# Kernel optimization log

Hardware: AMD Instinct MI355X
Metric: run time of the kernel (lower is better)

The kernel has to match this reference:

```python
import jax, jax.numpy as jnp
import numpy as np

B, C, H, W = 8, 512, 64, 64


def conv3x3(x, w, b):
    # x: [B,C,H,W], w: [O,I,3,3], b: [O]; stride 1, padding 1 (SAME)
    y = jax.lax.conv_general_dilated(
        x, w, window_strides=(1, 1), padding='SAME',
        dimension_numbers=('NCHW', 'OIHW', 'NCHW'))
    return y + b[None, :, None, None]


def setup_inputs() -> dict:
    key = jax.random.key(0)
    ks = jax.random.split(key, 8)
    wscale = 1.0 / np.sqrt(C * 9)  # keep attention logits in a sane range
    x = jax.random.normal(ks[0], (B, C, H, W), dtype=jnp.float32)
    wq = jax.random.normal(ks[1], (C, C, 3, 3), dtype=jnp.float32) * wscale
    bq = jax.random.normal(ks[2], (C,), dtype=jnp.float32) * 0.01
    wk = jax.random.normal(ks[3], (C, C, 3, 3), dtype=jnp.float32) * wscale
    bk = jax.random.normal(ks[4], (C,), dtype=jnp.float32) * 0.01
    wv = jax.random.normal(ks[5], (C, C, 3, 3), dtype=jnp.float32) * wscale
    bv = jax.random.normal(ks[6], (C,), dtype=jnp.float32) * 0.01
    gamma = jax.random.normal(ks[7], (1,), dtype=jnp.float32)
    return {'x': x, 'wq': wq, 'bq': bq, 'wk': wk, 'bk': bk,
            'wv': wv, 'bv': bv, 'gamma': gamma}


def reference(x, wq, bq, wk, bk, wv, bv, gamma):
    b, c, h, w = x.shape
    n = h * w
    q = conv3x3(x, wq, bq).reshape(b, c, n)   # [B,C,N]
    k = conv3x3(x, wk, bk).reshape(b, c, n)   # [B,C,N]
    v = conv3x3(x, wv, bv).reshape(b, c, n)   # [B,C,N]
    # channel-wise attention: [B,C,N] x [B,N,C] -> [B,C,C]
    attn = jnp.einsum('bcn,bdn->bcd', q, k)
    attn = jax.nn.softmax(attn, axis=-1)
    out = jnp.einsum('bcd,bdn->bcn', attn, v).reshape(b, c, h, w)
    return gamma * out + x
```

## Files before the change

### kernel.cpp

```cpp
#include <hip/hip_runtime.h>
#include <stdint.h>

typedef __attribute__((ext_vector_type(8))) short bf16x8;
typedef __attribute__((ext_vector_type(4))) float f32x4;
typedef __attribute__((ext_vector_type(4))) int i32x4;
typedef __attribute__((ext_vector_type(8))) int i32x8;
typedef __attribute__((ext_vector_type(8))) unsigned short u16x8;
typedef __attribute__((ext_vector_type(4))) unsigned short u16x4;

#define DI static __device__ __forceinline__

constexpr int CB = 8;
constexpr int BCH = 4;
constexpr int CC = 512;
constexpr int CN = 4096;
constexpr int K1 = CC * 9;
constexpr int MR = 3 * CC;
constexpr int KSPL = 8;
constexpr size_t XSPLIT = (size_t)BCH * 66 * 66 * 512;

DI unsigned short f2bf(float f) {
  union { float f; uint32_t u; } v; v.f = f;
  uint32_t r = (v.u + 0x7FFFu + ((v.u >> 16) & 1u)) >> 16;
  return (unsigned short)r;
}
DI float bf2f(unsigned short h) {
  union { uint32_t u; float f; } v; v.u = ((uint32_t)h) << 16;
  return v.f;
}
DI unsigned char f2e4m3(float x) {
  union { float f; uint32_t u; } v; v.f = x;
  uint32_t sgn = (v.u >> 24) & 0x80u;
  float a = fabsf(x);
  if (a < 0.015625f) {
    int qi = (int)rintf(a * 512.f);
    return (unsigned char)(sgn | (uint32_t)qi);
  }
  int e = (int)((v.u >> 23) & 0xff) - 127;
  uint32_t m3 = (v.u >> 20) & 7u;
  uint32_t rest = v.u & 0xFFFFFu;
  if (rest > 0x80000u || (rest == 0x80000u && (m3 & 1u))) {
    if (++m3 == 8u) { m3 = 0; ++e; }
  }
  if (e > 8 || (e == 8 && m3 == 7u)) return (unsigned char)(sgn | 0x7Eu);
  return (unsigned char)(sgn | ((uint32_t)(e + 7) << 3) | m3);
}

DI void g2lds16(const void* g, void* l) {
  __builtin_amdgcn_global_load_lds((const __attribute__((address_space(1))) void*)g,
                                   (__attribute__((address_space(3))) void*)l, 16, 0, 0);
}
#define SBAR()  __builtin_amdgcn_s_barrier()
#define SCHED() __builtin_amdgcn_sched_barrier(0)

__global__ __launch_bounds__(256) void pad_zero(unsigned short* __restrict__ Xhi,
                                                unsigned char* __restrict__ X8) {
  int id = blockIdx.x * 256 + threadIdx.x;
  if (id >= 4 * 260 * 16) return;
  int t = id & 15;
  int pp = (id >> 4) % 260;
  int b = id / (260 * 16);
  int hh, ww;
  if (pp < 66)       { hh = 0;  ww = pp; }
  else if (pp < 132) { hh = 65; ww = pp - 66; }
  else if (pp < 196) { hh = pp - 131; ww = 0; }
  else               { hh = pp - 195; ww = 65; }
  size_t pix = (((size_t)b * 66 + hh) * 66 + ww) * 512 + (size_t)t * 32;
  const u16x8 z = {0, 0, 0, 0, 0, 0, 0, 0};
  *(u16x8*)&Xhi[pix] = z;  *(u16x8*)&Xhi[pix + 8] = z;
  *(u16x8*)&Xhi[pix + 16] = z;  *(u16x8*)&Xhi[pix + 24] = z;
  const i32x4 z4 = {0, 0, 0, 0};
  *(i32x4*)&X8[pix] = z4;  *(i32x4*)&X8[pix + 16] = z4;
  *(i32x4*)&X8[XSPLIT + pix] = z4;  *(i32x4*)&X8[XSPLIT + pix + 16] = z4;
}

__global__ __launch_bounds__(256) void prep_xpad(const float* __restrict__ x,
                                                 unsigned short* __restrict__ Xhi,
                                                 unsigned char* __restrict__ X8) {
  int tid = threadIdx.x;
  int w = tid & 63;
  int ccl = tid >> 6;
  int blk = blockIdx.x;
  int h = blk & 63;
  int ccg = (blk >> 6) & 15;
  int b = blk >> 10;
  int c0 = (ccg * 4 + ccl) * 8;
  const float* xp = x + ((size_t)b * CC) * CN + h * 64 + w;
  u16x8 hi;
  unsigned long long lo8 = 0, hi8 = 0;
#pragma unroll
  for (int j = 0; j < 8; ++j) {
    float v = xp[(size_t)(c0 + j) * CN];
    unsigned short h16 = f2bf(v);
    float vhi = bf2f(h16);
    hi[j] = f2bf(vhi * 128.f);
    lo8 |= (unsigned long long)f2e4m3((v - vhi) * 256.f) << (8 * j);
    hi8 |= (unsigned long long)f2e4m3(vhi) << (8 * j);
  }
  size_t pix = (((size_t)b * 66 + (h + 1)) * 66 + (w + 1)) * 512;
  *(u16x8*)&Xhi[pix + c0] = hi;
  *(unsigned long long*)&X8[pix + c0] = lo8;
  *(unsigned long long*)&X8[XSPLIT + pix + c0] = hi8;
}

__global__ __launch_bounds__(256) void prep_abig(
    const float* __restrict__ wq, const float* __restrict__ wk,
    const float* __restrict__ wv, const float* __restrict__ bq,
    const float* __restrict__ bk, const float* __restrict__ bv,
    unsigned short* __restrict__ Ahi, unsigned char* __restrict__ A8,
    float* __restrict__ bias) {
  unsigned id = blockIdx.x * 256 + threadIdx.x;
  int m = id / K1;
  int r = id - m * K1;
  int t = r >> 9;
  int c = r & 511;
  int ky = t / 3;
  int kx = t - ky * 3;
  size_t ip = (size_t)m * 9216 + r;
  if (m < 1024) {
    const float* wp = (m < 512) ? wq : wk;
    int mm = (m < 512) ? m : m - 512;
    float wval = wp[(((size_t)mm * 512 + c) * 3 + ky) * 3 + kx];
    float whi = bf2f(f2bf(wval));
    Ahi[id] = f2bf(whi * 128.f);
    A8[ip] = f2e4m3(whi * 64.f);
    A8[ip + 4608] = f2e4m3((wval - whi) * 16384.f);
  } else {
    float wval = wv[(((size_t)(m - 1024) * 512 + c) * 3 + ky) * 3 + kx];
    Ahi[id] = f2bf(wval * 128.f);
    A8[ip] = 0;
    A8[ip + 4608] = 0;
  }
  if (id < 1536) {
    int mm = (int)id;
    bias[mm] = (mm < 512) ? bq[mm] : (mm < 1024) ? bk[mm - 512] : bv[mm - 1024];
  }
}

__global__ __launch_bounds__(512, 2) void conv_k(
    const unsigned short* __restrict__ Ahi,
    const unsigned char* __restrict__ A8,
    const unsigned short* __restrict__ Xhi,
    const unsigned char* __restrict__ X8,
    const float* __restrict__ bias,
    unsigned short* __restrict__ Qhi, unsigned short* __restrict__ Qlo,
    unsigned short* __restrict__ Khi, unsigned short* __restrict__ Klo,
    unsigned short* __restrict__ Vt)
{
  __shared__ __align__(16) unsigned char smem[4 * 32768];
  const int tid = threadIdx.x;
  const int lane = tid & 63;
  const int wid = tid >> 6;
  const int wr = wid >> 2;
  const int wc = wid & 3;

  int orig = blockIdx.x;
  int xcd, nbl, m0;
  if (orig < 256) {
    xcd = orig & 7; int j = orig >> 3;
    nbl = j >> 2;
    m0 = (j & 3) * 256;
  } else {
    int o = orig - 256;
    xcd = o & 7; int j = o >> 3;
    nbl = j >> 2;
    m0 = 1024 + (j & 3) * 128;
  }
  const int nb = xcd * 8 + nbl;
  const int n0 = nb * 256;
  const int bidx = n0 >> 12;
  const int nl0 = n0 & (CN - 1);
  const int h0 = nl0 >> 6;

  const int srow = tid >> 2;
  const int scu = tid & 3;
  const int scuS = scu ^ ((srow >> 1) & 3);
  const int d8 = (scuS & 1) ? -16 : 16;
  const size_t pixOfs = (((size_t)(bidx * 66 + h0 + (srow >> 6))) * 66 + (srow & 63)) * 512;
  const unsigned short* gAh0 = Ahi + (size_t)(m0 + srow) * K1 + scuS * 8;
  const unsigned short* gAh1 = gAh0 + (size_t)128 * K1;
  const unsigned short* gBh0 = Xhi + pixOfs + scuS * 8;
  const unsigned short* gBh1 = gBh0 + (size_t)2 * 66 * 512;
  const unsigned char* gA80 = A8 + (size_t)(m0 + srow) * 9216 + scuS * 16;
  const unsigned char* gA81 = gA80 + (size_t)128 * 9216;
  const unsigned char* gB80 = X8 + pixOfs + scuS * 16;
  const unsigned char* gB81 = gB80 + (size_t)2 * 66 * 512;
  const int wofs = wid * 1024;

  int c0S = 0, kxS = 0, tapS = 0;
  size_t tapOfs = 0;
  auto stage1 = [&](int slot) {
    int aOfs = tapS * 512 + c0S;
    size_t bOfs = tapOfs + (size_t)c0S;
    unsigned char* lA = smem + slot * 32768 + wofs;
    unsigned char* lB = smem + slot * 32768 + 16384 + wofs;
    g2lds16(gAh0 + aOfs, lA);
    g2lds16(gAh1 + aOfs, lA + 8192);
    g2lds16(gBh0 + bOfs, lB);
    g2lds16(gBh1 + bOfs, lB + 8192);
    c0S += 32;
    if (c0S == 512) {
      c0S = 0; ++tapS;
      if (kxS == 2) { kxS = 0; tapOfs += (size_t)64 * 512; }
      else { ++kxS; tapOfs += 512; }
    }
  };
  auto stage1v = [&](int slot) {
    int aOfs = tapS * 512 + c0S;
    size_t bOfs = tapOfs + (size_t)c0S;
    unsigned char* lA = smem + slot * 32768 + wofs;
    unsigned char* lB = smem + slot * 32768 + 16384 + wofs;
    g2lds16(gAh0 + aOfs, lA);
    g2lds16(gBh0 + bOfs, lB);
    g2lds16(gBh1 + bOfs, lB + 8192);
    c0S += 32;
    if (c0S == 512) {
      c0S = 0; ++tapS;
      if (kxS == 2) { kxS = 0; tapOfs += (size_t)64 * 512; }
      else { ++kxS; tapOfs += 512; }
    }
  };
  int c8 = 0, kx8 = 0, tap8 = 0, s8 = 0;
  size_t tapOfs8 = 0;
  auto stage2 = [&](int slot) {
    int so = (slot & 1) ? d8 : 0;
    int aOfs = s8 * 4608 + tap8 * 512 + c8;
    size_t bOfs = (size_t)s8 * XSPLIT + tapOfs8 + (size_t)c8;
    unsigned char* lA = smem + slot * 32768 + wofs;
    unsigned char* lB = smem + slot * 32768 + 16384 + wofs;
    g2lds16(gA80 + aOfs + so, lA);
    g2lds16(gA81 + aOfs + so, lA + 8192);
    g2lds16(gB80 + bOfs + so, lB);
    g2lds16(gB81 + bOfs + so, lB + 8192);
    c8 += 64;
    if (c8 == 512) {
      c8 = 0; ++tap8;
      if (tap8 == 9) { tap8 = 0; kx8 = 0; tapOfs8 = 0; ++s8; }
      else if (kx8 == 2) { kx8 = 0; tapOfs8 += (size_t)64 * 512; }
      else { ++kx8; tapOfs8 += 512; }
    }
  };

  f32x4 acc[8][4];
  const f32x4 fz = {0.f, 0.f, 0.f, 0.f};
#pragma unroll
  for (int i = 0; i < 8; ++i)
#pragma unroll
    for (int j = 0; j < 4; ++j) acc[i][j] = fz;

  const int kq = (lane >> 4) * 16;
  int slotC, slotS, t2;

  if (m0 < 1024) {
    const int rA = wr * 128 + (lane & 15);
    const int rB = wc * 64 + (lane & 15);
    const int kqA = kq ^ (((rA >> 1) & 3) << 4);
    const int kqB = kq ^ (((rB >> 1) & 3) << 4);

    stage1(0);
    stage1(1);
    asm volatile("s_waitcnt vmcnt(4)" ::: "memory");
    SCHED(); SBAR(); SCHED();
    {
      bf16x8 afA[4], bfA[4], afB[4], bfB[4], af1[4];
#pragma unroll
      for (int mf = 0; mf < 4; ++mf)
        afA[mf] = *(const bf16x8*)(smem + (rA + mf * 16) * 64 + kqA);
#pragma unroll
      for (int nf = 0; nf < 4; ++nf)
        bfA[nf] = *(const bf16x8*)(smem + 16384 + (rB + nf * 16) * 64 + kqB);
      slotC = 0; slotS = 2; t2 = 2;

#define CONV_BF(CURA, CURB, NXTA, NXTB)                                       \
  {                                                                           \
    if (t2 < 144) {                                                           \
      stage1(slotS); slotS = (slotS + 1) & 3;                                 \
      asm volatile("s_waitcnt vmcnt(4)" ::: "memory");                        \
    } else {                                                                  \
      asm volatile("s_waitcnt vmcnt(0)" ::: "memory");                        \
    }                                                                         \
    SCHED(); SBAR(); SCHED();                                                 \
    const unsigned char* lA = smem + slotC * 32768;                           \
    const int slotN = (slotC + 1) & 3;                                        \
    const unsigned char* lAn = smem + slotN * 32768;                          \
    _Pragma("unroll")                                                         \
    for (int mf = 0; mf < 4; ++mf)                                            \
      af1[mf] = *(const bf16x8*)(lA + (rA + 64 + mf * 16) * 64 + kqA);        \
    __builtin_amdgcn_s_setprio(1);                                            \
    _Pragma("unroll")                                                         \
    for (int mf = 0; mf < 4; ++mf) {                                          \
      _Pragma("unroll")                                                       \
      for (int nf = 0; nf < 4; ++nf)                                          \
        acc[mf][nf] = __builtin_amdgcn_mfma_f32_16x16x32_bf16(                \
            CURA[mf], CURB[nf], acc[mf][nf], 0, 0, 0);                        \
    }                                                                         \
    __builtin_amdgcn_s_setprio(0);                                            \
    _Pragma("unroll")                                                         \
    for (int mf = 0; mf < 4; ++mf)                                            \
      NXTA[mf] = *(const bf16x8*)(lAn + (rA + mf * 16) * 64 + kqA);           \
    _Pragma("unroll")                                                         \
    for (int nf = 0; nf < 4; ++nf)                                            \
      NXTB[nf] = *(const bf16x8*)(lAn + 16384 + (rB + nf * 16) * 64 + kqB);   \
    __builtin_amdgcn_s_setprio(1);                                            \
    _Pragma("unroll")                                                         \
    for (int mf = 0; mf < 4; ++mf) {                                          \
      _Pragma("unroll")                                                       \
      for (int nf = 0; nf < 4; ++nf)                                          \
        acc[mf + 4][nf] = __builtin_amdgcn_mfma_f32_16x16x32_bf16(            \
            af1[mf], CURB[nf], acc[mf + 4][nf], 0, 0, 0);                     \
    }                                                                         \
    __builtin_amdgcn_s_setprio(0);                                            \
    slotC = slotN;                                                            \
    ++t2;                                                                     \
  }

      for (int t = 0; t < 144; t += 2) {
        CONV_BF(afA, bfA, afB, bfB)
        CONV_BF(afB, bfB, afA, bfA)
      }
#undef CONV_BF
    }

    stage2(0); stage2(1);
    SCHED(); SBAR(); SCHED();
    stage2(2); stage2(3);
    {
      const int gq = lane >> 4;
      const int slotByte = (gq >> 1) << 15;
      const int cb2 = (gq & 1) * 2;
      const int fx = (((lane & 15) >> 1) & 3) ^ (gq >> 1);
      const int bo0 = ((cb2 ^ fx) << 4);
      const int bo1 = (((cb2 + 1) ^ fx) << 4);
      const int aRow = wr * 128 + (lane & 15);
      const int bRow = wc * 64 + (lane & 15);
      i32x8 aF[4], bF[4];
      for (int p = 0; p < 72; ++p) {
        SCHED(); SBAR(); SCHED();
        if (p < 71) { asm volatile("s_waitcnt vmcnt(8)" ::: "memory"); }
        else        { asm volatile("s_waitcnt vmcnt(0)" ::: "memory"); }
        SCHED();
        const unsigned char* pbA = smem + ((p & 1) << 16) + slotByte + aRow * 64;
        const unsigned char* pbB = smem + ((p & 1) << 16) + slotByte + 16384 + bRow * 64;
#pragma unroll
        for (int t = 0; t < 4; ++t) {
          *(i32x4*)&bF[t] = *(const i32x4*)(pbB + t * 1024 + bo0);
          *((i32x4*)&bF[t] + 1) = *(const i32x4*)(pbB + t * 1024 + bo1);
        }
#pragma unroll
        for (int s = 0; s < 4; ++s) {
          *(i32x4*)&aF[s] = *(const i32x4*)(pbA + s * 1024 + bo0);
          *((i32x4*)&aF[s] + 1) = *(const i32x4*)(pbA + s * 1024 + bo1);
        }
        __builtin_amdgcn_s_setprio(1);
#pragma unroll
        for (int s = 0; s < 4; ++s)
#pragma unroll
          for (int t = 0; t < 4; ++t)
            acc[s][t] = __builtin_amdgcn_mfma_scale_f32_16x16x128_f8f6f4(
                aF[s], bF[t], acc[s][t], 0, 0, 0, 127, 0, 127);
        __builtin_amdgcn_s_setprio(0);
#pragma unroll
        for (int s = 0; s < 4; ++s) {
          *(i32x4*)&aF[s] = *(const i32x4*)(pbA + (4 + s) * 1024 + bo0);
          *((i32x4*)&aF[s] + 1) = *(const i32x4*)(pbA + (4 + s) * 1024 + bo1);
        }
        __builtin_amdgcn_s_setprio(1);
#pragma unroll
        for (int s = 0; s < 4; ++s)
#pragma unroll
          for (int t = 0; t < 4; ++t)
            acc[s + 4][t] = __builtin_amdgcn_mfma_scale_f32_16x16x128_f8f6f4(
                aF[s], bF[t], acc[s + 4][t], 0, 0, 0, 127, 0, 127);
        __builtin_amdgcn_s_setprio(0);
        SCHED(); SBAR(); SCHED();
        if (p + 2 < 72) { stage2(2 * (p & 1)); stage2(2 * (p & 1) + 1); }
      }
    }
  } else {
    const int rAv = wr * 64 + (lane & 15);
    const int rB = wc * 64 + (lane & 15);
    const int kqA = kq ^ (((rAv >> 1) & 3) << 4);
    const int kqB = kq ^ (((rB >> 1) & 3) << 4);

    stage1v(0);
    stage1v(1);
    asm volatile("s_waitcnt vmcnt(3)" ::: "memory");
    SCHED(); SBAR(); SCHED();
    bf16x8 afA[4], bfA[4], afB[4], bfB[4];
#pragma unroll
    for (int mf = 0; mf < 4; ++mf)
      afA[mf] = *(const bf16x8*)(smem + (rAv + mf * 16) * 64 + kqA);
#pragma unroll
    for (int nf = 0; nf < 4; ++nf)
      bfA[nf] = *(const bf16x8*)(smem + 16384 + (rB + nf * 16) * 64 + kqB);
    slotC = 0; slotS = 2; t2 = 2;

#define CONV_LV(CURA, CURB, NXTA, NXTB)                                       \
  {                                                                           \
    if (t2 < 144) {                                                           \
      stage1v(slotS); slotS = (slotS + 1) & 3;                                \
      asm volatile("s_waitcnt vmcnt(3)" ::: "memory");                        \
    } else {                                                                  \
      asm volatile("s_waitcnt vmcnt(0)" ::: "memory");                        \
    }                                                                         \
    SCHED(); SBAR(); SCHED();                                                 \
    const int slotN = (slotC + 1) & 3;                                        \
    const unsigned char* lAn = smem + slotN * 32768;                          \
    _Pragma("unroll")                                                         \
    for (int mf = 0; mf < 4; ++mf)                                            \
      NXTA[mf] = *(const bf16x8*)(lAn + (rAv + mf * 16) * 64 + kqA);          \
    _Pragma("unroll")                                                         \
    for (int nf = 0; nf < 4; ++nf)                                            \
      NXTB[nf] = *(const bf16x8*)(lAn + 16384 + (rB + nf * 16) * 64 + kqB);   \
    __builtin_amdgcn_s_setprio(1);                                            \
    _Pragma("unroll")                                                         \
    for (int mf = 0; mf < 4; ++mf) {                                          \
      _Pragma("unroll")                                                       \
      for (int nf = 0; nf < 4; ++nf)                                          \
        acc[mf][nf] = __builtin_amdgcn_mfma_f32_16x16x32_bf16(                \
            CURA[mf], CURB[nf], acc[mf][nf], 0, 0, 0);                        \
    }                                                                         \
    __builtin_amdgcn_s_setprio(0);                                            \
    slotC = slotN;                                                            \
    ++t2;                                                                     \
  }

    for (int t = 0; t < 144; t += 2) {
      CONV_LV(afA, bfA, afB, bfB)
      CONV_LV(afB, bfB, afA, bfA)
    }
#undef CONV_LV
  }

  constexpr float SC = 1.f / 16384.f;
  if (m0 < 1024) {
#pragma unroll
    for (int mf = 0; mf < 8; ++mf) {
#pragma unroll
      for (int nf = 0; nf < 4; ++nf) {
        f32x4 a = acc[mf][nf];
        int mrow = m0 + wr * 128 + mf * 16 + ((lane >> 4) << 2);
        int ncol = nl0 + wc * 64 + nf * 16 + (lane & 15);
        if (m0 < 512) {
#pragma unroll
          for (int j = 0; j < 4; ++j) {
            float v = a[j] * SC + bias[mrow + j];
            unsigned short h16 = f2bf(v);
            size_t o = ((size_t)bidx * CC + (mrow + j)) * CN + ncol;
            Qhi[o] = h16;
            Qlo[o] = f2bf(v - bf2f(h16));
          }
        } else {
#pragma unroll
          for (int j = 0; j < 4; ++j) {
            float v = a[j] * SC + bias[mrow + j];
            unsigned short h16 = f2bf(v);
            size_t o = ((size_t)bidx * CC + (mrow + j - 512)) * CN + ncol;
            Khi[o] = h16;
            Klo[o] = f2bf(v - bf2f(h16));
          }
        }
      }
    }
  } else {
#pragma unroll
    for (int mf = 0; mf < 4; ++mf) {
#pragma unroll
      for (int nf = 0; nf < 4; ++nf) {
        f32x4 a = acc[mf][nf];
        int mrow = m0 + wr * 64 + mf * 16 + ((lane >> 4) << 2);
        int ncol = nl0 + wc * 64 + nf * 16 + (lane & 15);
        u16x4 vs;
#pragma unroll
        for (int j = 0; j < 4; ++j) vs[j] = f2bf(a[j] * SC + bias[mrow + j]);
        *(u16x4*)&Vt[((size_t)bidx * CN + ncol) * CC + (mrow - 1024)] = vs;
      }
    }
  }
}

DI int sofs(int row, int kb) { return row * 128 + (kb ^ ((row & 7) << 4)); }

template<int MODE>
__global__ __launch_bounds__(256) void gemm_k(
    const unsigned short* __restrict__ Qhi, const unsigned short* __restrict__ Qlo,
    const unsigned short* __restrict__ Khi, const unsigned short* __restrict__ Klo,
    const unsigned short* __restrict__ Vt,
    float* __restrict__ attn,
    const unsigned short* __restrict__ P,
    const float* __restrict__ xin,
    const float* __restrict__ gamma,
    float* __restrict__ out)
{
  __shared__ __align__(16) unsigned char sA[16384];
  __shared__ __align__(16) unsigned char sB[16384];
  const int tid = threadIdx.x;
  const int lane = tid & 63;
  const int wav = tid >> 6;
  const int wr = wav >> 1, wc = wav & 1;

  int m0, n0, bidx, Kbeg = 0, Kend, ks = 0;
  if constexpr (MODE == 1) {
    int tile = blockIdx.x & 15;
    ks = blockIdx.x >> 4;
    m0 = (tile & 3) * 128;
    n0 = (tile >> 2) * 128;
    bidx = blockIdx.z;
    Kbeg = ks * (3 * CN / KSPL);
    Kend = Kbeg + (3 * CN / KSPL);
  } else {
    m0 = (blockIdx.x & 3) * 128;
    n0 = (blockIdx.x >> 2) * 128;
    bidx = blockIdx.z;
    Kend = CC;
  }

  auto stage = [&](int k0) {
#pragma unroll
    for (int q = 0; q < 4; ++q) {
      int ci = q * 256 + tid;
      int row = ci >> 3;
      int ke = ((ci & 7) ^ (row & 7)) * 8;
      const unsigned short* ap;
      const unsigned short* bp;
      if constexpr (MODE == 1) {
        int ph = k0 >> 12;
        int kin = k0 & (CN - 1);
        const unsigned short* Aq = (ph == 2) ? Qlo : Qhi;
        const unsigned short* Bk = (ph == 1) ? Klo : Khi;
        ap = Aq + ((size_t)bidx * CC + (m0 + row)) * CN + (kin + ke);
        bp = Bk + ((size_t)bidx * CC + (n0 + row)) * CN + (kin + ke);
      } else {
        ap = P + ((size_t)bidx * CC + (m0 + row)) * CC + (k0 + ke);
        bp = Vt + ((size_t)bidx * CN + (n0 + row)) * CC + (k0 + ke);
      }
      int wbase = (q * 256 + wav * 64) * 16;
      g2lds16(ap, sA + wbase);
      g2lds16(bp, sB + wbase);
    }
  };

  f32x4 acc[4][4];
  const f32x4 fz = {0.f, 0.f, 0.f, 0.f};
#pragma unroll
  for (int i = 0; i < 4; ++i)
#pragma unroll
    for (int j = 0; j < 4; ++j) acc[i][j] = fz;

  for (int k0 = Kbeg; k0 < Kend; k0 += 64) {
    stage(k0);
    __syncthreads();
#pragma unroll
    for (int kkp = 0; kkp < 2; ++kkp) {
      bf16x8 af[4], bfv[4];
#pragma unroll
      for (int mf = 0; mf < 4; ++mf)
        af[mf] = *(const bf16x8*)&sA[sofs(wr * 64 + mf * 16 + (lane & 15),
                                          kkp * 64 + (lane >> 4) * 16)];
#pragma unroll
      for (int nf = 0; nf < 4; ++nf)
        bfv[nf] = *(const bf16x8*)&sB[sofs(wc * 64 + nf * 16 + (lane & 15),
                                           kkp * 64 + (lane >> 4) * 16)];
#pragma unroll
      for (int mf = 0; mf < 4; ++mf)
#pragma unroll
        for (int nf = 0; nf < 4; ++nf)
          acc[mf][nf] = __builtin_amdgcn_mfma_f32_16x16x32_bf16(
              af[mf], bfv[nf], acc[mf][nf], 0, 0, 0);
    }
    __syncthreads();
  }

  float g = 0.f;
  if constexpr (MODE == 2) g = gamma[0];
#pragma unroll
  for (int mf = 0; mf < 4; ++mf) {
#pragma unroll
    for (int nf = 0; nf < 4; ++nf) {
      f32x4 a = acc[mf][nf];
      int mrow = m0 + wr * 64 + mf * 16 + ((lane >> 4) << 2);
      int ncol = n0 + wc * 64 + nf * 16 + (lane & 15);
      if constexpr (MODE == 1) {
        size_t pbase = (size_t)ks * ((size_t)BCH * CC * CC);
#pragma unroll
        for (int j = 0; j < 4; ++j)
          attn[pbase + ((size_t)bidx * CC + (mrow + j)) * CC + ncol] = a[j];
      } else {
#pragma unroll
        for (int j = 0; j < 4; ++j) {
          size_t o = ((size_t)bidx * CC + (mrow + j)) * CN + ncol;
          out[o] = g * a[j] + xin[o];
        }
      }
    }
  }
}

__global__ __launch_bounds__(256) void softmax_k(const float* __restrict__ attn,
                                                 unsigned short* __restrict__ P) {
  int row = blockIdx.x * 4 + (threadIdx.x >> 6);
  int lane = threadIdx.x & 63;
  constexpr size_t PS = (size_t)BCH * CC * CC;
  const float* rp = attn + (size_t)row * 512 + lane * 8;
  f32x4 a = {0.f, 0.f, 0.f, 0.f};
  f32x4 b = {0.f, 0.f, 0.f, 0.f};
#pragma unroll
  for (int ksp = 0; ksp < KSPL; ++ksp) {
    a += *(const f32x4*)(rp + (size_t)ksp * PS);
    b += *(const f32x4*)(rp + (size_t)ksp * PS + 4);
  }
  float mx = fmaxf(fmaxf(fmaxf(a[0], a[1]), fmaxf(a[2], a[3])),
                   fmaxf(fmaxf(b[0], b[1]), fmaxf(b[2], b[3])));
#pragma unroll
  for (int s = 32; s > 0; s >>= 1) mx = fmaxf(mx, __shfl_xor(mx, s, 64));
  float e[8];
  float sum = 0.f;
#pragma unroll
  for (int j = 0; j < 4; ++j) { e[j] = __expf(a[j] - mx); sum += e[j]; }
#pragma unroll
  for (int j = 0; j < 4; ++j) { e[4 + j] = __expf(b[j] - mx); sum += e[4 + j]; }
#pragma unroll
  for (int s = 32; s > 0; s >>= 1) sum += __shfl_xor(sum, s, 64);
  float inv = 1.0f / sum;
  u16x8 o;
#pragma unroll
  for (int j = 0; j < 8; ++j) o[j] = f2bf(e[j] * inv);
  *(u16x8*)&P[(size_t)row * 512 + lane * 8] = o;
}

__global__ __launch_bounds__(256) void fill_sentinel(float* __restrict__ out, int n) {
  int i = blockIdx.x * 256 + threadIdx.x;
  if (i < n) out[i] = 1.0e4f;
}

extern "C" void kernel_launch(void* const* d_in, const int* in_sizes, int n_in,
                              void* d_out, int out_size, void* d_ws, size_t ws_size,
                              hipStream_t stream) {
  (void)in_sizes; (void)n_in;
  const float* x  = (const float*)d_in[0];
  const float* wq = (const float*)d_in[1];
  const float* bq = (const float*)d_in[2];
  const float* wk = (const float*)d_in[3];
  const float* bk = (const float*)d_in[4];
  const float* wv = (const float*)d_in[5];
  const float* bv = (const float*)d_in[6];
  const float* gm = (const float*)d_in[7];
  float* out = (float*)d_out;

  uint8_t* wsp = (uint8_t*)d_ws;
  auto take = [&](size_t bytes) {
    uint8_t* p = wsp;
    wsp += (bytes + 255) & ~(size_t)255;
    return p;
  };
  unsigned short* Xhi = (unsigned short*)take(XSPLIT * 2);
  unsigned char*  X8  = (unsigned char*)take(2 * XSPLIT);
  unsigned short* Ahi = (unsigned short*)take((size_t)MR * K1 * 2);
  unsigned char*  A8  = (unsigned char*)take((size_t)MR * 2 * K1);
  float* bias         = (float*)take((size_t)MR * 4);
  unsigned short* Khi = (unsigned short*)take((size_t)BCH * CC * CN * 2);
  unsigned short* Klo = (unsigned short*)take((size_t)BCH * CC * CN * 2);
  unsigned short* Vt  = (unsigned short*)take((size_t)BCH * CN * CC * 2);
  float* attn         = (float*)Xhi;
  unsigned short* P   = (unsigned short*)((uint8_t*)Xhi +
                          (size_t)KSPL * BCH * CC * CC * 4 + 256);

  size_t needed = (size_t)(wsp - (uint8_t*)d_ws);
  if (ws_size < needed) {
    fill_sentinel<<<(out_size + 255) / 256, 256, 0, stream>>>(out, out_size);
    return;
  }

  for (int ch = 0; ch < CB / BCH; ++ch) {
    const float* xch = x + (size_t)ch * BCH * CC * CN;
    float* outch = out + (size_t)ch * BCH * CC * CN;
    unsigned short* Qhi = (unsigned short*)outch;
    unsigned short* Qlo = Qhi + (size_t)BCH * CC * CN;

    pad_zero<<<(4 * 260 * 16 + 255) / 256, 256, 0, stream>>>(Xhi, X8);
    prep_xpad<<<BCH * 16 * 64, 256, 0, stream>>>(xch, Xhi, X8);
    if (ch == 0)
      prep_abig<<<(MR * K1) / 256, 256, 0, stream>>>(wq, wk, wv, bq, bk, bv,
                                                     Ahi, A8, bias);
    conv_k<<<dim3(512), 512, 0, stream>>>(Ahi, A8, Xhi, X8, bias,
                                          Qhi, Qlo, Khi, Klo, Vt);
    gemm_k<1><<<dim3(16 * KSPL, 1, BCH), 256, 0, stream>>>(Qhi, Qlo, Khi, Klo, Vt,
                                                           attn, P, xch, gm, outch);
    softmax_k<<<BCH * 128, 256, 0, stream>>>(attn, P);
    gemm_k<2><<<dim3(128, 1, BCH), 256, 0, stream>>>(Qhi, Qlo, Khi, Klo, Vt,
                                                     attn, P, xch, gm, outch);
  }
}
```

Before: 963.2 us.

## Split QK GEMM into dedicated kernel with 4-stage LDS pipeline and 128x256 tiles

Replaces the templated QK mode of the shared GEMM kernel with a dedicated qk_k kernel. It uses 512 threads, 128x256 output tiles, a 4-slot async global-to-LDS ring buffer with register double-buffered fragments, and s_setprio around the MFMA block. Blocks are also remapped across the K-split for locality. The goal is to hide load latency and remove the sync-per-step stalls of the simple stage/compute loop, at the cost of 96KB of LDS per block, which limits occupancy.

```diff
diff --git a/kernel.cpp b/kernel.cpp
--- a/kernel.cpp
+++ b/kernel.cpp
@@ -479,14 +479,130 @@
   }
 }
 
-DI int sofs(int row, int kb) { return row * 128 + (kb ^ ((row & 7) << 4)); }
-
-template<int MODE>
-__global__ __launch_bounds__(256) void gemm_k(
+__global__ __launch_bounds__(512, 2) void qk_k(
     const unsigned short* __restrict__ Qhi, const unsigned short* __restrict__ Qlo,
     const unsigned short* __restrict__ Khi, const unsigned short* __restrict__ Klo,
+    float* __restrict__ attn)
+{
+  __shared__ __align__(16) unsigned char smem[4 * 24576];
+  const int tid = threadIdx.x;
+  const int lane = tid & 63;
+  const int wid = tid >> 6;
+  const int wr = wid >> 2;
+  const int wc = wid & 3;
+
+  int orig = blockIdx.x;
+  int work = (orig & 7) * 8 + (orig >> 3);
+  const int mt = work & 3;
+  const int nt = (work >> 2) & 1;
+  const int ks = work >> 3;
+  const int bidx = blockIdx.z;
+  const int m0 = mt * 128;
+  const int n0 = nt * 256;
+
+  const int srow = tid >> 2;
+  const int scu = tid & 3;
+  const int scuS = scu ^ ((srow >> 1) & 3);
+  const size_t rowA = ((size_t)bidx * CC + m0 + srow) * CN + scuS * 8;
+  const size_t rowB = ((size_t)bidx * CC + n0 + srow) * CN + scuS * 8;
+  const size_t rowB2 = rowB + (size_t)128 * CN;
+  const int wofs = wid * 1024;
+
+  int kk = ks * 1536;
+  auto stageQ = [&](int slot) {
+    int ph = kk >> 12;
+    int kin = kk & (CN - 1);
+    const unsigned short* Aq = (ph == 2) ? Qlo : Qhi;
+    const unsigned short* Bk = (ph == 1) ? Klo : Khi;
+    unsigned char* lA = smem + slot * 24576 + wofs;
+    unsigned char* lB = smem + slot * 24576 + 8192 + wofs;
+    g2lds16(Aq + rowA + kin, lA);
+    g2lds16(Bk + rowB + kin, lB);
+    g2lds16(Bk + rowB2 + kin, lB + 8192);
+    kk += 32;
+  };
+
+  f32x4 acc[4][4];
+  const f32x4 fz = {0.f, 0.f, 0.f, 0.f};
+#pragma unroll
+  for (int i = 0; i < 4; ++i)
+#pragma unroll
+    for (int j = 0; j < 4; ++j) acc[i][j] = fz;
+
+  const int rAv = wr * 64 + (lane & 15);
+  const int rB = wc * 64 + (lane & 15);
+  const int kq = (lane >> 4) * 16;
+  const int kqA = kq ^ (((rAv >> 1) & 3) << 4);
+  const int kqB = kq ^ (((rB >> 1) & 3) << 4);
+
+  stageQ(0);
+  stageQ(1);
+  asm volatile("s_waitcnt vmcnt(3)" ::: "memory");
+  SCHED(); SBAR(); SCHED();
+  bf16x8 afA[4], bfA[4], afB[4], bfB[4];
+#pragma unroll
+  for (int mf = 0; mf < 4; ++mf)
+    afA[mf] = *(const bf16x8*)(smem + (rAv + mf * 16) * 64 + kqA);
+#pragma unroll
+  for (int nf = 0; nf < 4; ++nf)
+    bfA[nf] = *(const bf16x8*)(smem + 8192 + (rB + nf * 16) * 64 + kqB);
+  int slotC = 0, slotS = 2, t2 = 2;
+
+#define QK_BODY(CURA, CURB, NXTA, NXTB)                                       \
+  {                                                                           \
+    if (t2 < 48) {                                                            \
+      stageQ(slotS); slotS = (slotS + 1) & 3;                                 \
+      asm volatile("s_waitcnt vmcnt(3)" ::: "memory");                        \
+    } else {                                                                  \
+      asm volatile("s_waitcnt vmcnt(0)" ::: "memory");                        \
+    }                                                                         \
+    SCHED(); SBAR(); SCHED();                                                 \
+    const int slotN = (slotC + 1) & 3;                                        \
+    const unsigned char* lAn = smem + slotN * 24576;                          \
+    _Pragma("unroll")                                                         \
+    for (int mf = 0; mf < 4; ++mf)                                            \
+      NXTA[mf] = *(const bf16x8*)(lAn + (rAv + mf * 16) * 64 + kqA);          \
+    _Pragma("unroll")                                                         \
+    for (int nf = 0; nf < 4; ++nf)                                            \
+      NXTB[nf] = *(const bf16x8*)(lAn + 8192 + (rB + nf * 16) * 64 + kqB);    \
+    __builtin_amdgcn_s_setprio(1);                                            \
+    _Pragma("unroll")                                                         \
+    for (int mf = 0; mf < 4; ++mf) {                                          \
+      _Pragma("unroll")                                                       \
+      for (int nf = 0; nf < 4; ++nf)                                          \
+        acc[mf][nf] = __builtin_amdgcn_mfma_f32_16x16x32_bf16(                \
+            CURA[mf], CURB[nf], acc[mf][nf], 0, 0, 0);                        \
+    }                                                                         \
+    __builtin_amdgcn_s_setprio(0);                                            \
+    slotC = slotN;                                                            \
+    ++t2;                                                                     \
+  }
+
+  for (int t = 0; t < 48; t += 2) {
+    QK_BODY(afA, bfA, afB, bfB)
+    QK_BODY(afB, bfB, afA, bfA)
+  }
+#undef QK_BODY
+
+  size_t pbase = (size_t)ks * ((size_t)BCH * CC * CC);
+#pragma unroll
+  for (int mf = 0; mf < 4; ++mf) {
+#pragma unroll
+    for (int nf = 0; nf < 4; ++nf) {
+      f32x4 a = acc[mf][nf];
+      int mrow = m0 + wr * 64 + mf * 16 + ((lane >> 4) << 2);
+      int ncol = n0 + wc * 64 + nf * 16 + (lane & 15);
+#pragma unroll
+      for (int j = 0; j < 4; ++j)
+        attn[pbase + ((size_t)bidx * CC + (mrow + j)) * CC + ncol] = a[j];
+    }
+  }
+}
+
+DI int sofs(int row, int kb) { return row * 128 + (kb ^ ((row & 7) << 4)); }
+
+__global__ __launch_bounds__(256) void pv_k(
     const unsigned short* __restrict__ Vt,
-    float* __restrict__ attn,
     const unsigned short* __restrict__ P,
     const float* __restrict__ xin,
     const float* __restrict__ gamma,
@@ -499,21 +615,9 @@
   const int wav = tid >> 6;
   const int wr = wav >> 1, wc = wav & 1;
 
-  int m0, n0, bidx, Kbeg = 0, Kend, ks = 0;
-  if constexpr (MODE == 1) {
-    int tile = blockIdx.x & 15;
-    ks = blockIdx.x >> 4;
-    m0 = (tile & 3) * 128;
-    n0 = (tile >> 2) * 128;
-    bidx = blockIdx.z;
-    Kbeg = ks * (3 * CN / KSPL);
-    Kend = Kbeg + (3 * CN / KSPL);
-  } else {
-    m0 = (blockIdx.x & 3) * 128;
-    n0 = (blockIdx.x >> 2) * 128;
-    bidx = blockIdx.z;
-    Kend = CC;
-  }
+  const int m0 = (blockIdx.x & 3) * 128;
+  const int n0 = (blockIdx.x >> 2) * 128;
+  const int bidx = blockIdx.z;
 
   auto stage = [&](int k0) {
 #pragma unroll
@@ -521,19 +625,8 @@
       int ci = q * 256 + tid;
       int row = ci >> 3;
       int ke = ((ci & 7) ^ (row & 7)) * 8;
-      const unsigned short* ap;
-      const unsigned short* bp;
-      if constexpr (MODE == 1) {
-        int ph = k0 >> 12;
-        int kin = k0 & (CN - 1);
-        const unsigned short* Aq = (ph == 2) ? Qlo : Qhi;
-        const unsigned short* Bk = (ph == 1) ? Klo : Khi;
-        ap = Aq + ((size_t)bidx * CC + (m0 + row)) * CN + (kin + ke);
-        bp = Bk + ((size_t)bidx * CC + (n0 + row)) * CN + (kin + ke);
-      } else {
-        ap = P + ((size_t)bidx * CC + (m0 + row)) * CC + (k0 + ke);
-        bp = Vt + ((size_t)bidx * CN + (n0 + row)) * CC + (k0 + ke);
-      }
+      const unsigned short* ap = P + ((size_t)bidx * CC + (m0 + row)) * CC + (k0 + ke);
+      const unsigned short* bp = Vt + ((size_t)bidx * CN + (n0 + row)) * CC + (k0 + ke);
       int wbase = (q * 256 + wav * 64) * 16;
       g2lds16(ap, sA + wbase);
       g2lds16(bp, sB + wbase);
@@ -547,7 +640,7 @@
 #pragma unroll
     for (int j = 0; j < 4; ++j) acc[i][j] = fz;
 
-  for (int k0 = Kbeg; k0 < Kend; k0 += 64) {
+  for (int k0 = 0; k0 < CC; k0 += 64) {
     stage(k0);
     __syncthreads();
 #pragma unroll
@@ -571,8 +664,7 @@
     __syncthreads();
   }
 
-  float g = 0.f;
-  if constexpr (MODE == 2) g = gamma[0];
+  float g = gamma[0];
 #pragma unroll
   for (int mf = 0; mf < 4; ++mf) {
 #pragma unroll
@@ -580,17 +672,10 @@
       f32x4 a = acc[mf][nf];
       int mrow = m0 + wr * 64 + mf * 16 + ((lane >> 4) << 2);
       int ncol = n0 + wc * 64 + nf * 16 + (lane & 15);
-      if constexpr (MODE == 1) {
-        size_t pbase = (size_t)ks * ((size_t)BCH * CC * CC);
-#pragma unroll
-        for (int j = 0; j < 4; ++j)
-          attn[pbase + ((size_t)bidx * CC + (mrow + j)) * CC + ncol] = a[j];
-      } else {
-#pragma unroll
-        for (int j = 0; j < 4; ++j) {
-          size_t o = ((size_t)bidx * CC + (mrow + j)) * CN + ncol;
-          out[o] = g * a[j] + xin[o];
-        }
+#pragma unroll
+      for (int j = 0; j < 4; ++j) {
+        size_t o = ((size_t)bidx * CC + (mrow + j)) * CN + ncol;
+        out[o] = g * a[j] + xin[o];
       }
     }
   }
@@ -684,10 +769,8 @@
                                                      Ahi, A8, bias);
     conv_k<<<dim3(512), 512, 0, stream>>>(Ahi, A8, Xhi, X8, bias,
                                           Qhi, Qlo, Khi, Klo, Vt);
-    gemm_k<1><<<dim3(16 * KSPL, 1, BCH), 256, 0, stream>>>(Qhi, Qlo, Khi, Klo, Vt,
-                                                           attn, P, xch, gm, outch);
+    qk_k<<<dim3(64, 1, BCH), 512, 0, stream>>>(Qhi, Qlo, Khi, Klo, attn);
     softmax_k<<<BCH * 128, 256, 0, stream>>>(attn, P);
-    gemm_k<2><<<dim3(128, 1, BCH), 256, 0, stream>>>(Qhi, Qlo, Khi, Klo, Vt,
-                                                     attn, P, xch, gm, outch);
-  }
-}
+    pv_k<<<dim3(128, 1, BCH), 256, 0, stream>>>(Vt, P, xch, gm, outch);
+  }
+}
```

After: 945.2 us. Within noise of the previous version (-1.9%).
